# Optimization experiments

Measured on AMD Instinct MI355X. Metric: run time of the kernel, lower is better.

The kernel has to match this reference:

```python
import jax, jax.numpy as jnp
import numpy as np

L, H, P = 32768, 512, 256


def setup_inputs() -> dict:
    key = jax.random.key(0)
    ks = jax.random.split(key, 9)
    sH = 1.0 / np.sqrt(H).astype(np.float32)
    sP = 1.0 / np.sqrt(P).astype(np.float32)
    return {
        "input_sequence": jax.random.normal(ks[0], (L, H), jnp.float32),
        "Lambda_re": jax.random.normal(ks[1], (P,), jnp.float32),
        "Lambda_im": jax.random.normal(ks[2], (P,), jnp.float32) * np.float32(np.pi),
        "B_re": jax.random.normal(ks[3], (P, H), jnp.float32) * sH,
        "B_im": jax.random.normal(ks[4], (P, H), jnp.float32) * sH,
        "C_re": jax.random.normal(ks[5], (H, P), jnp.float32) * sP,
        "C_im": jax.random.normal(ks[6], (H, P), jnp.float32) * sP,
        "D": jax.random.normal(ks[7], (H,), jnp.float32),
        "log_step": jax.random.normal(ks[8], (P,), jnp.float32) - 3.0,
    }


def reference(input_sequence, Lambda_re, Lambda_im, B_re, B_im, C_re, C_im, D, log_step):
    # clip_eigs=True: enforce left-half-plane eigenvalues
    Lambda = jnp.clip(Lambda_re, None, -1e-4) + 1j * Lambda_im          # (P,)
    B_tilde = B_re + 1j * B_im                                          # (P,H)
    C_tilde = C_re + 1j * C_im                                          # (H,P)
    step = jnp.exp(log_step)                                            # step_rescale = 1.0, (P,)

    # ZOH discretization
    Lambda_bar = jnp.exp(Lambda * step)                                 # (P,) complex64
    B_bar = ((Lambda_bar - 1.0) / Lambda)[:, None] * B_tilde            # (P,H) complex64

    # Bu_elements: (L,P) complex; equivalent to vmap(lambda u: B_bar @ u)
    Bu = input_sequence.astype(B_bar.dtype) @ B_bar.T                   # (L,P)
    Lambda_elems = jnp.broadcast_to(Lambda_bar, (input_sequence.shape[0], Lambda_bar.shape[0]))

    def binop(q_i, q_j):
        A_i, b_i = q_i
        A_j, b_j = q_j
        return A_j * A_i, A_j * b_i + b_j

    _, xs = jax.lax.associative_scan(binop, (Lambda_elems, Bu))         # xs: (L,P)

    # conj_sym=True: ys = 2 * Re(C_tilde @ x) per step
    ys = 2.0 * (xs @ C_tilde.T).real                                    # (L,H)
    return ys + D * input_sequence
```

## Files before the change

kernel.cpp:

```cpp
#include <hip/hip_runtime.h>
#include <cstdint>
#include <cstddef>

typedef __bf16 bf16x8 __attribute__((ext_vector_type(8)));
typedef float f32x4 __attribute__((ext_vector_type(4)));

#define L_SEQ 32768
#define H_DIM 512
#define P_DIM 256
#define NP2   512
#define CHUNK 32
#define NCHUNK 1024
#define NSUPER 32

__device__ __forceinline__ void gload_lds16(const void* g, void* l) {
    __builtin_amdgcn_global_load_lds(
        (const __attribute__((address_space(1))) void*)g,
        (__attribute__((address_space(3))) void*)l,
        16, 0, 0);
}

__global__ void setup_kernel(const float* __restrict__ Lre, const float* __restrict__ Lim,
                             const float* __restrict__ lstep,
                             const float* __restrict__ Bre, const float* __restrict__ Bim,
                             const float* __restrict__ Cre, const float* __restrict__ Cim,
                             const float4* __restrict__ uin,
                             float* __restrict__ par,
                             __bf16* __restrict__ Bt, __bf16* __restrict__ Ct,
                             bf16x8* __restrict__ Ubf) {
    int b = blockIdx.x;
    if (b == 0) {
        int p = threadIdx.x;
        float lr = fminf(Lre[p], -1e-4f);
        float li = Lim[p];
        float st = expf(lstep[p]);
        float ldr = lr * st;
        float ldi = li * st;
        float er = expf(ldr);
        par[p]        = er * cosf(ldi);
        par[256 + p]  = er * sinf(ldi);
        float e32  = expf((float)CHUNK * ldr);
        float ph32 = (float)CHUNK * ldi;
        par[1024 + p] = e32 * cosf(ph32);
        par[1280 + p] = e32 * sinf(ph32);
        par[1536 + p] = ldr;
        par[1792 + p] = ldi;
    } else if (b <= 1024) {
        int bb = b - 1;
        if (bb < 512) {
            int idx = bb * 256 + threadIdx.x;
            int p = idx >> 9;
            float lr = fminf(Lre[p], -1e-4f);
            float li = Lim[p];
            float st = expf(lstep[p]);
            float er = expf(lr * st);
            float ar = er * cosf(li * st);
            float ai = er * sinf(li * st);
            float den = lr * lr + li * li;
            float mr = ar - 1.0f, mi = ai;
            float cr = (mr * lr + mi * li) / den;
            float ci = (mi * lr - mr * li) / den;
            float br = Bre[idx], bi = Bim[idx];
            int h = idx & 511;
            Bt[(size_t)p * NP2 + h]         = (__bf16)(cr * br - ci * bi);
            Bt[(size_t)(256 + p) * NP2 + h] = (__bf16)(cr * bi + ci * br);
        } else {
            int idx = (bb - 512) * 256 + threadIdx.x;
            int h = idx >> 8;
            int q = idx & 255;
            Ct[(size_t)h * NP2 + q]       = (__bf16)( 2.0f * Cre[idx]);
            Ct[(size_t)h * NP2 + 256 + q] = (__bf16)(-2.0f * Cim[idx]);
        }
    } else {
        int i = (b - 1025) * 256 + threadIdx.x;
        float4 a = uin[2 * i], c = uin[2 * i + 1];
        bf16x8 v;
        v[0] = (__bf16)a.x; v[1] = (__bf16)a.y; v[2] = (__bf16)a.z; v[3] = (__bf16)a.w;
        v[4] = (__bf16)c.x; v[5] = (__bf16)c.y; v[6] = (__bf16)c.z; v[7] = (__bf16)c.w;
        Ubf[i] = v;
    }
}

template<bool FUSE>
__global__ __launch_bounds__(256)
void gemm_bt_kernel(const __bf16* __restrict__ A, const __bf16* __restrict__ Bt,
                    void* __restrict__ CoutV, const float* __restrict__ Dvec,
                    const __bf16* __restrict__ Ubf) {
    const int K = NP2, N = NP2;
    __shared__ __align__(16) __bf16 As[3][128 * 64];
    __shared__ __align__(16) __bf16 Bs[2][128 * 64];
    const int t = threadIdx.x;
    const int l = t & 63;
    const int w = t >> 6;
    const int wr = w >> 1, wc = w & 1;
    const int b    = blockIdx.x;
    const int n_sw = (b & 7) * 128 + (b >> 3);
    const int row0 = (n_sw >> 2) * 128;
    const int col0 = (n_sw & 3) * 128;
    const int lr = l & 15;
    const int lk = (l >> 4) * 8;
    f32x4 acc[4][4] = {};

    auto STAGE_A = [&](int buf, int k0) {
#pragma unroll
        for (int i = 0; i < 4; ++i) {
            int off = i * 256 + t;
            int r  = off >> 3;
            int ce = ((off & 7) ^ (r & 7)) * 8;
            gload_lds16(A + (size_t)(row0 + r) * K + (k0 + ce), &As[buf][off * 8]);
        }
    };
    auto STAGE_B = [&](int buf, int k0) {
#pragma unroll
        for (int i = 0; i < 4; ++i) {
            int off = i * 256 + t;
            int r  = off >> 3;
            int ce = ((off & 7) ^ (r & 7)) * 8;
            gload_lds16(Bt + (size_t)(col0 + r) * K + (k0 + ce), &Bs[buf][off * 8]);
        }
    };

    auto COMPUTE = [&](int ba, int bb) {
#pragma unroll
        for (int kk = 0; kk < 64; kk += 32) {
            bf16x8 a[4], b2[4];
            const int ls = (kk + lk) >> 3;
#pragma unroll
            for (int m = 0; m < 4; ++m) {
                int row = wr * 64 + m * 16 + lr;
                a[m] = *reinterpret_cast<const bf16x8*>(&As[ba][row * 64 + ((ls ^ (row & 7)) << 3)]);
            }
#pragma unroll
            for (int n = 0; n < 4; ++n) {
                int row = wc * 64 + n * 16 + lr;
                b2[n] = *reinterpret_cast<const bf16x8*>(&Bs[bb][row * 64 + ((ls ^ (row & 7)) << 3)]);
            }
            __builtin_amdgcn_s_setprio(1);
#pragma unroll
            for (int m = 0; m < 4; ++m)
#pragma unroll
                for (int n = 0; n < 4; ++n)
                    acc[m][n] = __builtin_amdgcn_mfma_f32_16x16x32_bf16(a[m], b2[n], acc[m][n], 0, 0, 0);
            __builtin_amdgcn_s_setprio(0);
        }
    };

    STAGE_A(0, 0);
    STAGE_B(0, 0);
    STAGE_A(1, 64);
#pragma unroll
    for (int ks = 0; ks < 8; ++ks) {
        if (ks + 1 < 8) STAGE_B((ks + 1) & 1, (ks + 1) * 64);
        if (ks + 2 < 8) STAGE_A((ks + 2) % 3, (ks + 2) * 64);
        if (ks <= 5)      { asm volatile("s_waitcnt vmcnt(12)" ::: "memory"); }
        else if (ks == 6) { asm volatile("s_waitcnt vmcnt(8)"  ::: "memory"); }
        else              { asm volatile("s_waitcnt vmcnt(0)"  ::: "memory"); }
        __builtin_amdgcn_s_barrier();
        __builtin_amdgcn_sched_barrier(0);
        COMPUTE(ks % 3, ks & 1);
        __builtin_amdgcn_sched_barrier(0);
        __builtin_amdgcn_s_barrier();
    }

    const int lg = (l >> 4) * 4;
#pragma unroll
    for (int m = 0; m < 4; ++m) {
#pragma unroll
        for (int n = 0; n < 4; ++n) {
            int col = col0 + wc * 64 + n * 16 + lr;
#pragma unroll
            for (int j = 0; j < 4; ++j) {
                int row = row0 + wr * 64 + m * 16 + lg + j;
                size_t o = (size_t)row * N + col;
                if (FUSE) {
                    ((float*)CoutV)[o] = acc[m][n][j] + Dvec[col] * (float)Ubf[o];
                } else {
                    ((__bf16*)CoutV)[o] = (__bf16)acc[m][n][j];
                }
            }
        }
    }
}

__global__ void scanA_kernel(const __bf16* __restrict__ Bu, const float* __restrict__ par,
                             float* __restrict__ Fr, float* __restrict__ Fi) {
    int g = blockIdx.x;
    int p = threadIdx.x;
    float ar = par[p], ai = par[256 + p];
    const __bf16* bu = Bu + (size_t)g * CHUNK * NP2;
    float xr = 0.f, xi = 0.f;
#pragma unroll 4
    for (int i = 0; i < CHUNK; ++i) {
        float br = (float)bu[i * NP2 + p];
        float bi = (float)bu[i * NP2 + 256 + p];
        float nr = fmaf(ar, xr, fmaf(-ai, xi, br));
        float ni = fmaf(ar, xi, fmaf( ai, xr, bi));
        xr = nr; xi = ni;
    }
    Fr[g * 256 + p] = xr;
    Fi[g * 256 + p] = xi;
}

__global__ void scanB1_kernel(const float* __restrict__ Fr, const float* __restrict__ Fi,
                              const float* __restrict__ par,
                              float* __restrict__ Lr, float* __restrict__ Li,
                              float* __restrict__ Tr, float* __restrict__ Ti) {
    int s = blockIdx.x;
    int p = threadIdx.x;
    float pr = par[1024 + p], pi = par[1280 + p];
    float er = 0.f, ei = 0.f;
    int base = s * 32;
#pragma unroll
    for (int j = 0; j < 32; ++j) {
        int g = base + j;
        Lr[g * 256 + p] = er;
        Li[g * 256 + p] = ei;
        float fr = Fr[g * 256 + p], fi = Fi[g * 256 + p];
        float nr = fmaf(pr, er, fmaf(-pi, ei, fr));
        float ni = fmaf(pr, ei, fmaf( pi, er, fi));
        er = nr; ei = ni;
    }
    Tr[s * 256 + p] = er;
    Ti[s * 256 + p] = ei;
}

__global__ void scanC_kernel(const __bf16* __restrict__ Bu, const float* __restrict__ par,
                             const float* __restrict__ Lr, const float* __restrict__ Li,
                             const float* __restrict__ Tr, const float* __restrict__ Ti,
                             __bf16* __restrict__ xs) {
    int g = blockIdx.x;
    int p = threadIdx.x;
    int s = g >> 5, k = g & 31;
    float ar = par[p], ai = par[256 + p];
    float ldr = par[1536 + p], ldi = par[1792 + p];
    float e1  = expf(1024.0f * ldr);
    float ph1 = 1024.0f * ldi;
    float q1r = e1 * cosf(ph1), q1i = e1 * sinf(ph1);
    float er = 0.f, ei = 0.f;
    for (int s2 = 0; s2 < s; ++s2) {
        float fr = Tr[s2 * 256 + p], fi = Ti[s2 * 256 + p];
        float nr = fmaf(q1r, er, fmaf(-q1i, ei, fr));
        float ni = fmaf(q1r, ei, fmaf( q1i, er, fi));
        er = nr; ei = ni;
    }
    float kk = (float)(32 * k);
    float e  = expf(kk * ldr);
    float ph = kk * ldi;
    float qr = e * cosf(ph), qi = e * sinf(ph);
    float lr0 = Lr[g * 256 + p], li0 = Li[g * 256 + p];
    float xr = fmaf(qr, er, fmaf(-qi, ei, lr0));
    float xi = fmaf(qr, ei, fmaf( qi, er, li0));
    const __bf16* bu = Bu + (size_t)g * CHUNK * NP2;
    __bf16* xo = xs + (size_t)g * CHUNK * NP2;
#pragma unroll 4
    for (int i = 0; i < CHUNK; ++i) {
        float br = (float)bu[i * NP2 + p];
        float bi = (float)bu[i * NP2 + 256 + p];
        float nr = fmaf(ar, xr, fmaf(-ai, xi, br));
        float ni = fmaf(ar, xi, fmaf( ai, xr, bi));
        xr = nr; xi = ni;
        xo[i * NP2 + p]       = (__bf16)xr;
        xo[i * NP2 + 256 + p] = (__bf16)xi;
    }
}

extern "C" void kernel_launch(void* const* d_in, const int* in_sizes, int n_in,
                              void* d_out, int out_size, void* d_ws, size_t ws_size,
                              hipStream_t stream) {
    const float* u   = (const float*)d_in[0];
    const float* Lre = (const float*)d_in[1];
    const float* Lim = (const float*)d_in[2];
    const float* Bre = (const float*)d_in[3];
    const float* Bim = (const float*)d_in[4];
    const float* Cre = (const float*)d_in[5];
    const float* Cim = (const float*)d_in[6];
    const float* Dv  = (const float*)d_in[7];
    const float* lst = (const float*)d_in[8];

    char* w = (char*)d_ws;
    size_t off = 0;
    float* par = (float*)(w + off);      off += 16 * 1024;
    __bf16* Btm = (__bf16*)(w + off);    off += (size_t)NP2 * NP2 * 2;
    __bf16* Ctm = (__bf16*)(w + off);    off += (size_t)NP2 * NP2 * 2;
    float* Fr  = (float*)(w + off);      off += (size_t)NCHUNK * 256 * 4;
    float* Fi  = (float*)(w + off);      off += (size_t)NCHUNK * 256 * 4;
    float* Lr  = (float*)(w + off);      off += (size_t)NCHUNK * 256 * 4;
    float* Li  = (float*)(w + off);      off += (size_t)NCHUNK * 256 * 4;
    float* Tr  = (float*)(w + off);      off += (size_t)NSUPER * 256 * 4;
    float* Ti  = (float*)(w + off);      off += (size_t)NSUPER * 256 * 4;
    __bf16* Ubf = (__bf16*)(w + off);    off += (size_t)L_SEQ * H_DIM * 2;
    __bf16* Xs  = (__bf16*)(w + off);    off += (size_t)L_SEQ * NP2 * 2;
    if (ws_size < off) return;

    __bf16* Bu = (__bf16*)d_out;

    setup_kernel  <<<9217, 256, 0, stream>>>(Lre, Lim, lst, Bre, Bim, Cre, Cim,
                                             (const float4*)u, par, Btm, Ctm, (bf16x8*)Ubf);
    gemm_bt_kernel<false><<<1024, 256, 0, stream>>>(Ubf, Btm, (void*)Bu, nullptr, nullptr);
    scanA_kernel  <<<NCHUNK, 256, 0, stream>>>(Bu, par, Fr, Fi);
    scanB1_kernel <<<NSUPER, 256, 0, stream>>>(Fr, Fi, par, Lr, Li, Tr, Ti);
    scanC_kernel  <<<NCHUNK, 256, 0, stream>>>(Bu, par, Lr, Li, Tr, Ti, Xs);
    gemm_bt_kernel<true><<<1024, 256, 0, stream>>>(Xs, Ctm, d_out, Dv, Ubf);
}
```

Baseline: 98.17 us.

## Stage GEMM epilogue through LDS and collapse three-pass scan into two kernels

The GEMM epilogue now writes accumulators into a padded LDS tile and re-reads them row-wise. Each thread can then issue contiguous float4/bf16x8 global stores and vector reads of Ubf and D, in place of scattered scalar stores. The chunked scan drops the superchunk pass (scanB1). Instead, each scanC block serially combines all previous chunk carries with the per-chunk decay power. The scan kernels now process two channels per thread with bf16x2 loads and stores and a packed float4 carry buffer. The cost is a serial loop of up to 1023 steps in late scanC blocks, plus shared-memory traffic and a block barrier in the GEMM epilogue.

```diff
diff --git a/kernel.cpp b/kernel.cpp
--- a/kernel.cpp
+++ b/kernel.cpp
@@ -3,6 +3,7 @@
 #include <cstddef>
 
 typedef __bf16 bf16x8 __attribute__((ext_vector_type(8)));
+typedef __bf16 bf16x2 __attribute__((ext_vector_type(2)));
 typedef float f32x4 __attribute__((ext_vector_type(4)));
 
 #define L_SEQ 32768
@@ -11,7 +12,6 @@
 #define NP2   512
 #define CHUNK 32
 #define NCHUNK 1024
-#define NSUPER 32
 
 __device__ __forceinline__ void gload_lds16(const void* g, void* l) {
     __builtin_amdgcn_global_load_lds(
@@ -43,8 +43,6 @@
         float ph32 = (float)CHUNK * ldi;
         par[1024 + p] = e32 * cosf(ph32);
         par[1280 + p] = e32 * sinf(ph32);
-        par[1536 + p] = ldr;
-        par[1792 + p] = ldi;
     } else if (b <= 1024) {
         int bb = b - 1;
         if (bb < 512) {
@@ -87,8 +85,9 @@
                     void* __restrict__ CoutV, const float* __restrict__ Dvec,
                     const __bf16* __restrict__ Ubf) {
     const int K = NP2, N = NP2;
-    __shared__ __align__(16) __bf16 As[3][128 * 64];
-    __shared__ __align__(16) __bf16 Bs[2][128 * 64];
+    __shared__ __align__(16) char pool[81920];
+    __bf16* Asp = (__bf16*)pool;
+    __bf16* Bsp = (__bf16*)(pool + 49152);
     const int t = threadIdx.x;
     const int l = t & 63;
     const int w = t >> 6;
@@ -107,7 +106,7 @@
             int off = i * 256 + t;
             int r  = off >> 3;
             int ce = ((off & 7) ^ (r & 7)) * 8;
-            gload_lds16(A + (size_t)(row0 + r) * K + (k0 + ce), &As[buf][off * 8]);
+            gload_lds16(A + (size_t)(row0 + r) * K + (k0 + ce), Asp + buf * 8192 + off * 8);
         }
     };
     auto STAGE_B = [&](int buf, int k0) {
@@ -116,7 +115,7 @@
             int off = i * 256 + t;
             int r  = off >> 3;
             int ce = ((off & 7) ^ (r & 7)) * 8;
-            gload_lds16(Bt + (size_t)(col0 + r) * K + (k0 + ce), &Bs[buf][off * 8]);
+            gload_lds16(Bt + (size_t)(col0 + r) * K + (k0 + ce), Bsp + buf * 8192 + off * 8);
         }
     };
 
@@ -128,12 +127,12 @@
 #pragma unroll
             for (int m = 0; m < 4; ++m) {
                 int row = wr * 64 + m * 16 + lr;
-                a[m] = *reinterpret_cast<const bf16x8*>(&As[ba][row * 64 + ((ls ^ (row & 7)) << 3)]);
+                a[m] = *reinterpret_cast<const bf16x8*>(Asp + ba * 8192 + row * 64 + ((ls ^ (row & 7)) << 3));
             }
 #pragma unroll
             for (int n = 0; n < 4; ++n) {
                 int row = wc * 64 + n * 16 + lr;
-                b2[n] = *reinterpret_cast<const bf16x8*>(&Bs[bb][row * 64 + ((ls ^ (row & 7)) << 3)]);
+                b2[n] = *reinterpret_cast<const bf16x8*>(Bsp + bb * 8192 + row * 64 + ((ls ^ (row & 7)) << 3));
             }
             __builtin_amdgcn_s_setprio(1);
 #pragma unroll
@@ -162,105 +161,116 @@
         __builtin_amdgcn_s_barrier();
     }
 
+    float* st = (float*)pool;
     const int lg = (l >> 4) * 4;
 #pragma unroll
-    for (int m = 0; m < 4; ++m) {
-#pragma unroll
-        for (int n = 0; n < 4; ++n) {
-            int col = col0 + wc * 64 + n * 16 + lr;
-#pragma unroll
-            for (int j = 0; j < 4; ++j) {
-                int row = row0 + wr * 64 + m * 16 + lg + j;
-                size_t o = (size_t)row * N + col;
-                if (FUSE) {
-                    ((float*)CoutV)[o] = acc[m][n][j] + Dvec[col] * (float)Ubf[o];
-                } else {
-                    ((__bf16*)CoutV)[o] = (__bf16)acc[m][n][j];
-                }
-            }
+    for (int m = 0; m < 4; ++m)
+#pragma unroll
+        for (int n = 0; n < 4; ++n)
+#pragma unroll
+            for (int j = 0; j < 4; ++j)
+                st[(wr * 64 + m * 16 + lg + j) * 132 + (wc * 64 + n * 16 + lr)] = acc[m][n][j];
+    __syncthreads();
+
+    const int row  = t >> 1;
+    const int half = t & 1;
+    const float* srow = st + row * 132 + half * 64;
+    const size_t gbase = (size_t)(row0 + row) * N + col0 + half * 64;
+    if (FUSE) {
+        float* out = (float*)CoutV;
+        const float* dv = Dvec + col0 + half * 64;
+#pragma unroll
+        for (int c = 0; c < 8; ++c) {
+            float4 v0 = *(const float4*)(srow + c * 8);
+            float4 v1 = *(const float4*)(srow + c * 8 + 4);
+            bf16x8 uv = *reinterpret_cast<const bf16x8*>(Ubf + gbase + c * 8);
+            float4 d0 = *(const float4*)(dv + c * 8);
+            float4 d1 = *(const float4*)(dv + c * 8 + 4);
+            float4 o0, o1;
+            o0.x = fmaf(d0.x, (float)uv[0], v0.x);
+            o0.y = fmaf(d0.y, (float)uv[1], v0.y);
+            o0.z = fmaf(d0.z, (float)uv[2], v0.z);
+            o0.w = fmaf(d0.w, (float)uv[3], v0.w);
+            o1.x = fmaf(d1.x, (float)uv[4], v1.x);
+            o1.y = fmaf(d1.y, (float)uv[5], v1.y);
+            o1.z = fmaf(d1.z, (float)uv[6], v1.z);
+            o1.w = fmaf(d1.w, (float)uv[7], v1.w);
+            *(float4*)(out + gbase + c * 8)     = o0;
+            *(float4*)(out + gbase + c * 8 + 4) = o1;
+        }
+    } else {
+        __bf16* out = (__bf16*)CoutV;
+#pragma unroll
+        for (int c = 0; c < 8; ++c) {
+            float4 v0 = *(const float4*)(srow + c * 8);
+            float4 v1 = *(const float4*)(srow + c * 8 + 4);
+            bf16x8 v;
+            v[0] = (__bf16)v0.x; v[1] = (__bf16)v0.y; v[2] = (__bf16)v0.z; v[3] = (__bf16)v0.w;
+            v[4] = (__bf16)v1.x; v[5] = (__bf16)v1.y; v[6] = (__bf16)v1.z; v[7] = (__bf16)v1.w;
+            *reinterpret_cast<bf16x8*>(out + gbase + c * 8) = v;
         }
     }
 }
 
 __global__ void scanA_kernel(const __bf16* __restrict__ Bu, const float* __restrict__ par,
-                             float* __restrict__ Fr, float* __restrict__ Fi) {
+                             float4* __restrict__ Fc) {
     int g = blockIdx.x;
-    int p = threadIdx.x;
-    float ar = par[p], ai = par[256 + p];
+    int t = threadIdx.x;
+    int p0 = 2 * t, p1 = 2 * t + 1;
+    float ar0 = par[p0], ai0 = par[256 + p0];
+    float ar1 = par[p1], ai1 = par[256 + p1];
     const __bf16* bu = Bu + (size_t)g * CHUNK * NP2;
-    float xr = 0.f, xi = 0.f;
+    float xr0 = 0.f, xi0 = 0.f, xr1 = 0.f, xi1 = 0.f;
 #pragma unroll 4
     for (int i = 0; i < CHUNK; ++i) {
-        float br = (float)bu[i * NP2 + p];
-        float bi = (float)bu[i * NP2 + 256 + p];
-        float nr = fmaf(ar, xr, fmaf(-ai, xi, br));
-        float ni = fmaf(ar, xi, fmaf( ai, xr, bi));
-        xr = nr; xi = ni;
-    }
-    Fr[g * 256 + p] = xr;
-    Fi[g * 256 + p] = xi;
-}
-
-__global__ void scanB1_kernel(const float* __restrict__ Fr, const float* __restrict__ Fi,
-                              const float* __restrict__ par,
-                              float* __restrict__ Lr, float* __restrict__ Li,
-                              float* __restrict__ Tr, float* __restrict__ Ti) {
-    int s = blockIdx.x;
-    int p = threadIdx.x;
-    float pr = par[1024 + p], pi = par[1280 + p];
-    float er = 0.f, ei = 0.f;
-    int base = s * 32;
-#pragma unroll
-    for (int j = 0; j < 32; ++j) {
-        int g = base + j;
-        Lr[g * 256 + p] = er;
-        Li[g * 256 + p] = ei;
-        float fr = Fr[g * 256 + p], fi = Fi[g * 256 + p];
-        float nr = fmaf(pr, er, fmaf(-pi, ei, fr));
-        float ni = fmaf(pr, ei, fmaf( pi, er, fi));
-        er = nr; ei = ni;
-    }
-    Tr[s * 256 + p] = er;
-    Ti[s * 256 + p] = ei;
+        bf16x2 re = *reinterpret_cast<const bf16x2*>(bu + i * NP2 + p0);
+        bf16x2 im = *reinterpret_cast<const bf16x2*>(bu + i * NP2 + 256 + p0);
+        float br0 = (float)re[0], br1 = (float)re[1];
+        float bi0 = (float)im[0], bi1 = (float)im[1];
+        float nr0 = fmaf(ar0, xr0, fmaf(-ai0, xi0, br0));
+        float ni0 = fmaf(ar0, xi0, fmaf( ai0, xr0, bi0));
+        float nr1 = fmaf(ar1, xr1, fmaf(-ai1, xi1, br1));
+        float ni1 = fmaf(ar1, xi1, fmaf( ai1, xr1, bi1));
+        xr0 = nr0; xi0 = ni0; xr1 = nr1; xi1 = ni1;
+    }
+    float4 f; f.x = xr0; f.y = xi0; f.z = xr1; f.w = xi1;
+    Fc[g * 128 + t] = f;
 }
 
 __global__ void scanC_kernel(const __bf16* __restrict__ Bu, const float* __restrict__ par,
-                             const float* __restrict__ Lr, const float* __restrict__ Li,
-                             const float* __restrict__ Tr, const float* __restrict__ Ti,
-                             __bf16* __restrict__ xs) {
+                             const float4* __restrict__ Fc, __bf16* __restrict__ xs) {
     int g = blockIdx.x;
-    int p = threadIdx.x;
-    int s = g >> 5, k = g & 31;
-    float ar = par[p], ai = par[256 + p];
-    float ldr = par[1536 + p], ldi = par[1792 + p];
-    float e1  = expf(1024.0f * ldr);
-    float ph1 = 1024.0f * ldi;
-    float q1r = e1 * cosf(ph1), q1i = e1 * sinf(ph1);
-    float er = 0.f, ei = 0.f;
-    for (int s2 = 0; s2 < s; ++s2) {
-        float fr = Tr[s2 * 256 + p], fi = Ti[s2 * 256 + p];
-        float nr = fmaf(q1r, er, fmaf(-q1i, ei, fr));
-        float ni = fmaf(q1r, ei, fmaf( q1i, er, fi));
-        er = nr; ei = ni;
-    }
-    float kk = (float)(32 * k);
-    float e  = expf(kk * ldr);
-    float ph = kk * ldi;
-    float qr = e * cosf(ph), qi = e * sinf(ph);
-    float lr0 = Lr[g * 256 + p], li0 = Li[g * 256 + p];
-    float xr = fmaf(qr, er, fmaf(-qi, ei, lr0));
-    float xi = fmaf(qr, ei, fmaf( qi, er, li0));
+    int t = threadIdx.x;
+    int p0 = 2 * t, p1 = 2 * t + 1;
+    float ar0 = par[p0], ai0 = par[256 + p0];
+    float ar1 = par[p1], ai1 = par[256 + p1];
+    float pr0 = par[1024 + p0], pi0 = par[1280 + p0];
+    float pr1 = par[1024 + p1], pi1 = par[1280 + p1];
+    float er0 = 0.f, ei0 = 0.f, er1 = 0.f, ei1 = 0.f;
+    for (int j = 0; j < g; ++j) {
+        float4 f = Fc[j * 128 + t];
+        float nr0 = fmaf(pr0, er0, fmaf(-pi0, ei0, f.x));
+        float ni0 = fmaf(pr0, ei0, fmaf( pi0, er0, f.y));
+        float nr1 = fmaf(pr1, er1, fmaf(-pi1, ei1, f.z));
+        float ni1 = fmaf(pr1, ei1, fmaf( pi1, er1, f.w));
+        er0 = nr0; ei0 = ni0; er1 = nr1; ei1 = ni1;
+    }
+    float xr0 = er0, xi0 = ei0, xr1 = er1, xi1 = ei1;
     const __bf16* bu = Bu + (size_t)g * CHUNK * NP2;
     __bf16* xo = xs + (size_t)g * CHUNK * NP2;
 #pragma unroll 4
     for (int i = 0; i < CHUNK; ++i) {
-        float br = (float)bu[i * NP2 + p];
-        float bi = (float)bu[i * NP2 + 256 + p];
-        float nr = fmaf(ar, xr, fmaf(-ai, xi, br));
-        float ni = fmaf(ar, xi, fmaf( ai, xr, bi));
-        xr = nr; xi = ni;
-        xo[i * NP2 + p]       = (__bf16)xr;
-        xo[i * NP2 + 256 + p] = (__bf16)xi;
+        bf16x2 re = *reinterpret_cast<const bf16x2*>(bu + i * NP2 + p0);
+        bf16x2 im = *reinterpret_cast<const bf16x2*>(bu + i * NP2 + 256 + p0);
+        float nr0 = fmaf(ar0, xr0, fmaf(-ai0, xi0, (float)re[0]));
+        float ni0 = fmaf(ar0, xi0, fmaf( ai0, xr0, (float)im[0]));
+        float nr1 = fmaf(ar1, xr1, fmaf(-ai1, xi1, (float)re[1]));
+        float ni1 = fmaf(ar1, xi1, fmaf( ai1, xr1, (float)im[1]));
+        xr0 = nr0; xi0 = ni0; xr1 = nr1; xi1 = ni1;
+        bf16x2 wre; wre[0] = (__bf16)xr0; wre[1] = (__bf16)xr1;
+        bf16x2 wim; wim[0] = (__bf16)xi0; wim[1] = (__bf16)xi1;
+        *reinterpret_cast<bf16x2*>(xo + i * NP2 + p0)       = wre;
+        *reinterpret_cast<bf16x2*>(xo + i * NP2 + 256 + p0) = wim;
     }
 }
 
@@ -282,12 +292,7 @@
     float* par = (float*)(w + off);      off += 16 * 1024;
     __bf16* Btm = (__bf16*)(w + off);    off += (size_t)NP2 * NP2 * 2;
     __bf16* Ctm = (__bf16*)(w + off);    off += (size_t)NP2 * NP2 * 2;
-    float* Fr  = (float*)(w + off);      off += (size_t)NCHUNK * 256 * 4;
-    float* Fi  = (float*)(w + off);      off += (size_t)NCHUNK * 256 * 4;
-    float* Lr  = (float*)(w + off);      off += (size_t)NCHUNK * 256 * 4;
-    float* Li  = (float*)(w + off);      off += (size_t)NCHUNK * 256 * 4;
-    float* Tr  = (float*)(w + off);      off += (size_t)NSUPER * 256 * 4;
-    float* Ti  = (float*)(w + off);      off += (size_t)NSUPER * 256 * 4;
+    float4* Fc = (float4*)(w + off);     off += (size_t)NCHUNK * 128 * 16;
     __bf16* Ubf = (__bf16*)(w + off);    off += (size_t)L_SEQ * H_DIM * 2;
     __bf16* Xs  = (__bf16*)(w + off);    off += (size_t)L_SEQ * NP2 * 2;
     if (ws_size < off) return;
@@ -297,8 +302,7 @@
     setup_kernel  <<<9217, 256, 0, stream>>>(Lre, Lim, lst, Bre, Bim, Cre, Cim,
                                              (const float4*)u, par, Btm, Ctm, (bf16x8*)Ubf);
     gemm_bt_kernel<false><<<1024, 256, 0, stream>>>(Ubf, Btm, (void*)Bu, nullptr, nullptr);
-    scanA_kernel  <<<NCHUNK, 256, 0, stream>>>(Bu, par, Fr, Fi);
-    scanB1_kernel <<<NSUPER, 256, 0, stream>>>(Fr, Fi, par, Lr, Li, Tr, Ti);
-    scanC_kernel  <<<NCHUNK, 256, 0, stream>>>(Bu, par, Lr, Li, Tr, Ti, Xs);
+    scanA_kernel  <<<NCHUNK, 128, 0, stream>>>(Bu, par, Fc);
+    scanC_kernel  <<<NCHUNK, 128, 0, stream>>>(Bu, par, Fc, Xs);
     gemm_bt_kernel<true><<<1024, 256, 0, stream>>>(Xs, Ctm, d_out, Dv, Ubf);
 }
```

Result: slower. 365.3 us (+272.1%).
